# Kernel tuning notes

Hardware: AMD Instinct MI355X
Metric: run time of the kernel (lower is better)

Reference implementation:

```python
import jax, jax.numpy as jnp
import numpy as np

N_QUBITS = 4
N_LAYERS = 3
N_OUTPUTS = 4
BATCH = 1048576


def _ry(t):
    # RY(t) = [[cos(t/2), -sin(t/2)], [sin(t/2), cos(t/2)]]; t may be scalar or (B,)
    c = jnp.cos(t / 2)
    s = jnp.sin(t / 2)
    m = jnp.stack([jnp.stack([c, -s], -1), jnp.stack([s, c], -1)], -2)
    return m.astype(jnp.complex64)


def _rx(t):
    c = jnp.cos(t / 2).astype(jnp.complex64)
    s = jnp.sin(t / 2).astype(jnp.complex64)
    return jnp.stack([jnp.stack([c, -1j * s], -1), jnp.stack([-1j * s, c], -1)], -2)


def _rz(t):
    e = jnp.exp(-1j * t.astype(jnp.complex64) / 2)  # exp(-i t/2)
    z = jnp.zeros_like(e)
    return jnp.stack([jnp.stack([e, z], -1), jnp.stack([z, jnp.conj(e)], -1)], -2)


def _apply_1q(state, U, q):
    # shared 2x2 gate U on wire q; state: (B, 2,2,2,2)
    s = jnp.moveaxis(state, q + 1, -1)
    s = jnp.einsum('ij,...j->...i', U, s)
    return jnp.moveaxis(s, -1, q + 1)


def _apply_1q_batched(state, U, q):
    # per-sample 2x2 gate U: (B,2,2) on wire q
    s = jnp.moveaxis(state, q + 1, -1)  # (B, ..., 2)
    s = jnp.einsum('bij,b...j->b...i', U, s)
    return jnp.moveaxis(s, -1, q + 1)


def _apply_cnot(state, c, t):
    s = jnp.moveaxis(state, (c + 1, t + 1), (-2, -1))  # (..., ctrl, tgt)
    s = jnp.stack([s[..., 0, :], s[..., 1, ::-1]], axis=-2)
    return jnp.moveaxis(s, (-2, -1), (c + 1, t + 1))


def setup_inputs() -> dict:
    key = jax.random.key(0)
    kx, kw = jax.random.split(key)
    x = jax.random.normal(kx, (BATCH, 2), dtype=jnp.float32)
    weights = jax.random.normal(kw, (N_LAYERS, N_QUBITS, 3), dtype=jnp.float32) * 0.1
    return {"x": x, "weights": weights}


def reference(x, weights):
    B = x.shape[0]
    # |0...0> state, batched
    state = jnp.zeros((B,) + (2,) * N_QUBITS, jnp.complex64)
    state = state.at[(slice(None),) + (0,) * N_QUBITS].set(1.0)
    # data encoding: RY(inputs[i % 2]) on wire i (per-sample angles)
    for i in range(N_QUBITS):
        state = _apply_1q_batched(state, _ry(x[:, i % 2]), i)
    # variational layers (shared angles)
    for l in range(N_LAYERS):
        for i in range(N_QUBITS):
            state = _apply_1q(state, _rx(weights[l, i, 0]), i)
            state = _apply_1q(state, _ry(weights[l, i, 1]), i)
            state = _apply_1q(state, _rz(weights[l, i, 2]), i)
        for i in range(N_QUBITS):
            state = _apply_cnot(state, i, (i + 1) % N_QUBITS)
    probs = state.real ** 2 + state.imag ** 2  # (B,2,2,2,2)
    outs = []
    for q in range(N_OUTPUTS):
        p = jnp.moveaxis(probs, q + 1, 1).reshape(B, 2, -1).sum(-1)
        outs.append(p[:, 0] - p[:, 1])  # <Z_q>
    return jnp.stack(outs, -1)  # (B, N_OUTPUTS)
```

## Files before the change

### kernel.cpp

```cpp
#include <hip/hip_runtime.h>
#include <hip/hip_bf16.h>


__global__ __launch_bounds__(256) void qnn_setup(const float* __restrict__ w,
                                                 float* __restrict__ C_out) {
    __shared__ float Ur[16][16];
    __shared__ float Ui[16][16];
    __shared__ float Csh[100];
    const int t = threadIdx.x;

    if (t < 100) Csh[t] = 0.0f;

    if (t < 16) {
        float ar[16], ai[16];
#pragma unroll
        for (int i = 0; i < 16; i++) { ar[i] = (i == t) ? 1.0f : 0.0f; ai[i] = 0.0f; }

#pragma unroll
        for (int l = 0; l < 3; l++) {
#pragma unroll
            for (int wq = 0; wq < 4; wq++) {
                const int st = 1 << (3 - wq);
                float th, s, c;
                th = w[(l * 4 + wq) * 3 + 0] * 0.5f;
                __sincosf(th, &s, &c);
#pragma unroll
                for (int lo = 0; lo < 16; lo++) if (!(lo & st)) {
                    const int hi = lo | st;
                    const float arl = ar[lo], ail = ai[lo], arh = ar[hi], aih = ai[hi];
                    ar[lo] = c * arl + s * aih;
                    ai[lo] = c * ail - s * arh;
                    ar[hi] = c * arh + s * ail;
                    ai[hi] = c * aih - s * arl;
                }
                th = w[(l * 4 + wq) * 3 + 1] * 0.5f;
                __sincosf(th, &s, &c);
#pragma unroll
                for (int lo = 0; lo < 16; lo++) if (!(lo & st)) {
                    const int hi = lo | st;
                    const float arl = ar[lo], ail = ai[lo], arh = ar[hi], aih = ai[hi];
                    ar[lo] = c * arl - s * arh;
                    ai[lo] = c * ail - s * aih;
                    ar[hi] = s * arl + c * arh;
                    ai[hi] = s * ail + c * aih;
                }
                th = w[(l * 4 + wq) * 3 + 2] * 0.5f;
                __sincosf(th, &s, &c);
#pragma unroll
                for (int lo = 0; lo < 16; lo++) if (!(lo & st)) {
                    const int hi = lo | st;
                    const float arl = ar[lo], ail = ai[lo], arh = ar[hi], aih = ai[hi];
                    ar[lo] = c * arl + s * ail;
                    ai[lo] = c * ail - s * arl;
                    ar[hi] = c * arh - s * aih;
                    ai[hi] = c * aih + s * arh;
                }
            }
#pragma unroll
            for (int ci = 0; ci < 4; ci++) {
                const int cst = 1 << (3 - ci);
                const int tst = 1 << (3 - ((ci + 1) & 3));
#pragma unroll
                for (int k = 0; k < 16; k++) if ((k & cst) && !(k & tst)) {
                    const int k2 = k | tst;
                    const float tr = ar[k], ti = ai[k];
                    ar[k] = ar[k2]; ai[k] = ai[k2];
                    ar[k2] = tr;    ai[k2] = ti;
                }
            }
        }
#pragma unroll
        for (int i = 0; i < 16; i++) { Ur[i][t] = ar[i]; Ui[i][t] = ai[i]; }
    }
    __syncthreads();

    {
        const int i = t >> 4;
        const int j = t & 15;
        float m0 = 0.f, m1 = 0.f, m2 = 0.f, m3 = 0.f;
#pragma unroll
        for (int k = 0; k < 16; k++) {
            const float r = Ur[k][i] * Ur[k][j] + Ui[k][i] * Ui[k][j];
            m0 += ((k >> 3) & 1) ? -r : r;
            m1 += ((k >> 2) & 1) ? -r : r;
            m2 += ((k >> 1) & 1) ? -r : r;
            m3 += ((k >> 0) & 1) ? -r : r;
        }
        const int mm = ((i >> 3) & 1) + ((i >> 1) & 1) + ((j >> 3) & 1) + ((j >> 1) & 1);
        const int nn = ((i >> 2) & 1) + (i & 1) + ((j >> 2) & 1) + (j & 1);
        atomicAdd(&Csh[0 * 25 + mm * 5 + nn], m0);
        atomicAdd(&Csh[1 * 25 + mm * 5 + nn], m1);
        atomicAdd(&Csh[2 * 25 + mm * 5 + nn], m2);
        atomicAdd(&Csh[3 * 25 + mm * 5 + nn], m3);
    }
    __syncthreads();
    if (t < 100) C_out[t] = Csh[t];
}

constexpr int SPT = 4;

__global__ __launch_bounds__(256) void qnn_batch(const float2* __restrict__ x,
                                                 const float* __restrict__ C,
                                                 float* __restrict__ out,
                                                 int B) {
    const int q = threadIdx.x & 3;

    float cf[25];
#pragma unroll
    for (int i = 0; i < 25; i++) cf[i] = C[q * 25 + i];

    const int s_in_block = threadIdx.x >> 2;
    const int base = blockIdx.x * (64 * SPT) + s_in_block;

    float2 xs[SPT];
#pragma unroll
    for (int k = 0; k < SPT; k++) {
        const int b = base + k * 64;
        xs[k] = (b < B) ? x[b] : make_float2(0.f, 0.f);
    }

#pragma unroll
    for (int k = 0; k < SPT; k++) {
        const int b = base + k * 64;
        if (b < B) {
            float s0, c0, s1, c1;
            __sincosf(xs[k].x * 0.5f, &s0, &c0);
            __sincosf(xs[k].y * 0.5f, &s1, &c1);
            const float cc0 = c0 * c0, ss0 = s0 * s0, cs0 = c0 * s0;
            const float cc1 = c1 * c1, ss1 = s1 * s1, cs1 = c1 * s1;
            const float p0[5] = { cc0 * cc0, cc0 * cs0, cs0 * cs0, cs0 * ss0, ss0 * ss0 };
            const float p1[5] = { cc1 * cc1, cc1 * cs1, cs1 * cs1, cs1 * ss1, ss1 * ss1 };
            float acc = 0.0f;
#pragma unroll
            for (int m = 0; m < 5; m++) {
                float inner = 0.0f;
#pragma unroll
                for (int n = 0; n < 5; n++)
                    inner = fmaf(cf[m * 5 + n], p1[n], inner);
                acc = fmaf(p0[m], inner, acc);
            }
            out[b * 4 + q] = acc;
        }
    }
}

extern "C" void kernel_launch(void* const* d_in, const int* in_sizes, int n_in,
                              void* d_out, int out_size, void* d_ws, size_t ws_size,
                              hipStream_t stream) {
    const float* x = (const float*)d_in[0];
    const float* w = (const float*)d_in[1];
    float* C = (float*)d_ws;
    const int B = in_sizes[0] / 2;

    qnn_setup<<<1, 256, 0, stream>>>(w, C);

    const int grid = (B + 64 * SPT - 1) / (64 * SPT);
    qnn_batch<<<grid, 256, 0, stream>>>((const float2*)x, C, (float*)d_out, B);
}
```

Baseline: 80.23 us.

## Fuse unitary setup into batch kernel with shuffle-parallel simulation and grid-stride loop

Merges the single-block setup kernel and the batch kernel into one launch. Every block recomputes the 16x16 unitary and the coefficient tables on its own, with each thread holding one amplitude and applying gates through wavefront xor-shuffles. The batch part becomes a grid-stride loop over a grid capped at 1024 blocks, prefetching the next x value. This removes the second launch and the round trip of the coefficients through global memory. In exchange every block repeats the setup work, and the capped grid gives fewer resident waves for hiding memory latency.

Result: no change. 80.74 us (+0.6%).

```diff
diff --git a/kernel.cpp b/kernel.cpp
--- a/kernel.cpp
+++ b/kernel.cpp
@@ -2,8 +2,10 @@
 #include <hip/hip_bf16.h>
 
 
-__global__ __launch_bounds__(256) void qnn_setup(const float* __restrict__ w,
-                                                 float* __restrict__ C_out) {
+__global__ __launch_bounds__(256, 4) void qnn_fused(const float2* __restrict__ x,
+                                                    const float* __restrict__ w,
+                                                    float* __restrict__ out,
+                                                    int B) {
     __shared__ float Ur[16][16];
     __shared__ float Ui[16][16];
     __shared__ float Csh[100];
@@ -11,66 +13,58 @@
 
     if (t < 100) Csh[t] = 0.0f;
 
-    if (t < 16) {
-        float ar[16], ai[16];
+    {
+        const int amp = t & 15;
+        const int col = t >> 4;
+        float ar = (amp == col) ? 1.0f : 0.0f;
+        float ai = 0.0f;
+
+        float wl[36];
 #pragma unroll
-        for (int i = 0; i < 16; i++) { ar[i] = (i == t) ? 1.0f : 0.0f; ai[i] = 0.0f; }
+        for (int i = 0; i < 36; i++) wl[i] = w[i];
 
 #pragma unroll
         for (int l = 0; l < 3; l++) {
 #pragma unroll
             for (int wq = 0; wq < 4; wq++) {
                 const int st = 1 << (3 - wq);
-                float th, s, c;
-                th = w[(l * 4 + wq) * 3 + 0] * 0.5f;
-                __sincosf(th, &s, &c);
-#pragma unroll
-                for (int lo = 0; lo < 16; lo++) if (!(lo & st)) {
-                    const int hi = lo | st;
-                    const float arl = ar[lo], ail = ai[lo], arh = ar[hi], aih = ai[hi];
-                    ar[lo] = c * arl + s * aih;
-                    ai[lo] = c * ail - s * arh;
-                    ar[hi] = c * arh + s * ail;
-                    ai[hi] = c * aih - s * arl;
+                float s, c;
+                __sincosf(wl[(l * 4 + wq) * 3 + 0] * 0.5f, &s, &c);
+                {
+                    const float pr = __shfl_xor(ar, st);
+                    const float pi = __shfl_xor(ai, st);
+                    const float nr = c * ar + s * pi;
+                    const float ni = c * ai - s * pr;
+                    ar = nr; ai = ni;
                 }
-                th = w[(l * 4 + wq) * 3 + 1] * 0.5f;
-                __sincosf(th, &s, &c);
-#pragma unroll
-                for (int lo = 0; lo < 16; lo++) if (!(lo & st)) {
-                    const int hi = lo | st;
-                    const float arl = ar[lo], ail = ai[lo], arh = ar[hi], aih = ai[hi];
-                    ar[lo] = c * arl - s * arh;
-                    ai[lo] = c * ail - s * aih;
-                    ar[hi] = s * arl + c * arh;
-                    ai[hi] = s * ail + c * aih;
+                __sincosf(wl[(l * 4 + wq) * 3 + 1] * 0.5f, &s, &c);
+                {
+                    const float pr = __shfl_xor(ar, st);
+                    const float pi = __shfl_xor(ai, st);
+                    const float sg = (amp & st) ? s : -s;
+                    const float nr = c * ar + sg * pr;
+                    const float ni = c * ai + sg * pi;
+                    ar = nr; ai = ni;
                 }
-                th = w[(l * 4 + wq) * 3 + 2] * 0.5f;
-                __sincosf(th, &s, &c);
-#pragma unroll
-                for (int lo = 0; lo < 16; lo++) if (!(lo & st)) {
-                    const int hi = lo | st;
-                    const float arl = ar[lo], ail = ai[lo], arh = ar[hi], aih = ai[hi];
-                    ar[lo] = c * arl + s * ail;
-                    ai[lo] = c * ail - s * arl;
-                    ar[hi] = c * arh - s * aih;
-                    ai[hi] = c * aih + s * arh;
+                __sincosf(wl[(l * 4 + wq) * 3 + 2] * 0.5f, &s, &c);
+                {
+                    const float sg = (amp & st) ? -s : s;
+                    const float nr = c * ar + sg * ai;
+                    const float ni = c * ai - sg * ar;
+                    ar = nr; ai = ni;
                 }
             }
 #pragma unroll
             for (int ci = 0; ci < 4; ci++) {
                 const int cst = 1 << (3 - ci);
                 const int tst = 1 << (3 - ((ci + 1) & 3));
-#pragma unroll
-                for (int k = 0; k < 16; k++) if ((k & cst) && !(k & tst)) {
-                    const int k2 = k | tst;
-                    const float tr = ar[k], ti = ai[k];
-                    ar[k] = ar[k2]; ai[k] = ai[k2];
-                    ar[k2] = tr;    ai[k2] = ti;
-                }
+                const float pr = __shfl_xor(ar, tst);
+                const float pi = __shfl_xor(ai, tst);
+                if (amp & cst) { ar = pr; ai = pi; }
             }
         }
-#pragma unroll
-        for (int i = 0; i < 16; i++) { Ur[i][t] = ar[i]; Ui[i][t] = ai[i]; }
+        Ur[amp][col] = ar;
+        Ui[amp][col] = ai;
     }
     __syncthreads();
 
@@ -94,53 +88,40 @@
         atomicAdd(&Csh[3 * 25 + mm * 5 + nn], m3);
     }
     __syncthreads();
-    if (t < 100) C_out[t] = Csh[t];
-}
 
-constexpr int SPT = 4;
-
-__global__ __launch_bounds__(256) void qnn_batch(const float2* __restrict__ x,
-                                                 const float* __restrict__ C,
-                                                 float* __restrict__ out,
-                                                 int B) {
-    const int q = threadIdx.x & 3;
-
+    const int q = t & 3;
     float cf[25];
 #pragma unroll
-    for (int i = 0; i < 25; i++) cf[i] = C[q * 25 + i];
+    for (int i = 0; i < 25; i++) cf[i] = Csh[q * 25 + i];
 
-    const int s_in_block = threadIdx.x >> 2;
-    const int base = blockIdx.x * (64 * SPT) + s_in_block;
+    const int s_loc = t >> 2;
+    const int stride = gridDim.x * 64;
+    int b = blockIdx.x * 64 + s_loc;
+    float2 xv = (b < B) ? x[b] : make_float2(0.f, 0.f);
+    while (b < B) {
+        const int bn = b + stride;
+        float2 xn = make_float2(0.f, 0.f);
+        if (bn < B) xn = x[bn];
 
-    float2 xs[SPT];
+        float s0, c0, s1, c1;
+        __sincosf(xv.x * 0.5f, &s0, &c0);
+        __sincosf(xv.y * 0.5f, &s1, &c1);
+        const float cc0 = c0 * c0, ss0 = s0 * s0, cs0 = c0 * s0;
+        const float cc1 = c1 * c1, ss1 = s1 * s1, cs1 = c1 * s1;
+        const float p0[5] = { cc0 * cc0, cc0 * cs0, cs0 * cs0, cs0 * ss0, ss0 * ss0 };
+        const float p1[5] = { cc1 * cc1, cc1 * cs1, cs1 * cs1, cs1 * ss1, ss1 * ss1 };
+        float acc = 0.0f;
 #pragma unroll
-    for (int k = 0; k < SPT; k++) {
-        const int b = base + k * 64;
-        xs[k] = (b < B) ? x[b] : make_float2(0.f, 0.f);
-    }
+        for (int m = 0; m < 5; m++) {
+            float inner = 0.0f;
+#pragma unroll
+            for (int n = 0; n < 5; n++)
+                inner = fmaf(cf[m * 5 + n], p1[n], inner);
+            acc = fmaf(p0[m], inner, acc);
+        }
+        out[b * 4 + q] = acc;
 
-#pragma unroll
-    for (int k = 0; k < SPT; k++) {
-        const int b = base + k * 64;
-        if (b < B) {
-            float s0, c0, s1, c1;
-            __sincosf(xs[k].x * 0.5f, &s0, &c0);
-            __sincosf(xs[k].y * 0.5f, &s1, &c1);
-            const float cc0 = c0 * c0, ss0 = s0 * s0, cs0 = c0 * s0;
-            const float cc1 = c1 * c1, ss1 = s1 * s1, cs1 = c1 * s1;
-            const float p0[5] = { cc0 * cc0, cc0 * cs0, cs0 * cs0, cs0 * ss0, ss0 * ss0 };
-            const float p1[5] = { cc1 * cc1, cc1 * cs1, cs1 * cs1, cs1 * ss1, ss1 * ss1 };
-            float acc = 0.0f;
-#pragma unroll
-            for (int m = 0; m < 5; m++) {
-                float inner = 0.0f;
-#pragma unroll
-                for (int n = 0; n < 5; n++)
-                    inner = fmaf(cf[m * 5 + n], p1[n], inner);
-                acc = fmaf(p0[m], inner, acc);
-            }
-            out[b * 4 + q] = acc;
-        }
+        b = bn; xv = xn;
     }
 }
 
@@ -149,11 +130,9 @@
                               hipStream_t stream) {
     const float* x = (const float*)d_in[0];
     const float* w = (const float*)d_in[1];
-    float* C = (float*)d_ws;
     const int B = in_sizes[0] / 2;
 
-    qnn_setup<<<1, 256, 0, stream>>>(w, C);
-
-    const int grid = (B + 64 * SPT - 1) / (64 * SPT);
-    qnn_batch<<<grid, 256, 0, stream>>>((const float2*)x, C, (float*)d_out, B);
+    int grid = (B + 63) / 64;
+    if (grid > 1024) grid = 1024;
+    qnn_fused<<<grid, 256, 0, stream>>>((const float2*)x, w, (float*)d_out, B);
 }
```
